# Optimization experiments

Hardware: AMD Instinct MI355X
Metric: run time of the kernel (lower is better)

The kernel has to match this reference:

```python
import jax, jax.numpy as jnp
import numpy as np

D_MODEL = 1024
NHEAD = 16
D_K = D_MODEL // NHEAD
D_FF = 4096
EPS = 1e-5


def _layer_norm(x, g, b):
    mu = jnp.mean(x, axis=-1, keepdims=True)
    var = jnp.mean(jnp.square(x - mu), axis=-1, keepdims=True)
    return (x - mu) * jax.lax.rsqrt(var + EPS) * g + b


def setup_inputs() -> dict:
    key = jax.random.key(0)
    ks = jax.random.split(key, 14)
    s = 0.02
    d = {
        'src': jax.random.normal(ks[0], (4, 2048, D_MODEL), dtype=jnp.float32),
        'Wq': jax.random.normal(ks[1], (D_MODEL, D_MODEL), dtype=jnp.float32) * s,
        'bq': jnp.zeros((D_MODEL,), jnp.float32),
        'Wk': jax.random.normal(ks[2], (D_MODEL, D_MODEL), dtype=jnp.float32) * s,
        'bk': jnp.zeros((D_MODEL,), jnp.float32),
        'Wv': jax.random.normal(ks[3], (D_MODEL, D_MODEL), dtype=jnp.float32) * s,
        'bv': jnp.zeros((D_MODEL,), jnp.float32),
        'Wo': jax.random.normal(ks[4], (D_MODEL, D_MODEL), dtype=jnp.float32) * s,
        'bo': jnp.zeros((D_MODEL,), jnp.float32),
        'W1': jax.random.normal(ks[5], (D_MODEL, D_FF), dtype=jnp.float32) * s,
        'b1': jnp.zeros((D_FF,), jnp.float32),
        'W2': jax.random.normal(ks[6], (D_FF, D_MODEL), dtype=jnp.float32) * s,
        'b2': jnp.zeros((D_MODEL,), jnp.float32),
        'ln1_g': jnp.ones((D_MODEL,), jnp.float32),
        'ln1_b': jnp.zeros((D_MODEL,), jnp.float32),
        'ln2_g': jnp.ones((D_MODEL,), jnp.float32),
        'ln2_b': jnp.zeros((D_MODEL,), jnp.float32),
    }
    return d


def reference(src, Wq, bq, Wk, bk, Wv, bv, Wo, bo, W1, b1, W2, b2,
              ln1_g, ln1_b, ln2_g, ln2_b):
    B, L, _ = src.shape
    # QKV projections -> [B, H, L, d_k]
    def heads(x, W, b):
        y = x @ W + b
        return y.reshape(B, L, NHEAD, D_K).transpose(0, 2, 1, 3)
    Q = heads(src, Wq, bq)
    K = heads(src, Wk, bk)
    V = heads(src, Wv, bv)
    # scores [B, H, Lq, Lk]
    scores = jnp.einsum('bhqd,bhkd->bhqk', Q, K) / jnp.sqrt(jnp.float32(D_K))
    attn = jax.nn.softmax(scores, axis=-1)
    ctx = jnp.einsum('bhqk,bhkd->bhqd', attn, V)
    ctx = ctx.transpose(0, 2, 1, 3).reshape(B, L, D_MODEL)
    attn_out = ctx @ Wo + bo
    x = _layer_norm(src + attn_out, ln1_g, ln1_b)
    ff = jax.nn.relu(x @ W1 + b1) @ W2 + b2
    return _layer_norm(x + ff, ln2_g, ln2_b)
```

## Files before the change

kernel.cpp:

```cpp
#include <hip/hip_runtime.h>
#include <hip/hip_bf16.h>


#define D_MODEL 1024
#define SEQ     2048
#define BATCH   4
#define NHEAD   16
#define D_FF    4096
#define M_ROWS  (BATCH * SEQ)

typedef __attribute__((ext_vector_type(8))) short bf16x8;
typedef __attribute__((ext_vector_type(4))) float f32x4;

__device__ __forceinline__ ushort f2bf(float x) {
    unsigned u = __float_as_uint(x);
    unsigned r = (u + 0x7FFFu + ((u >> 16) & 1u)) >> 16;
    return (ushort)r;
}

__device__ __forceinline__ int swz_off(int r, int q) {
    return ((r >> 1) << 6) | (((((r & 1) << 2) | q) ^ ((r >> 1) & 7)) << 3);
}

__global__ __launch_bounds__(256) void cast_kernel(
    const float* __restrict__ x, ushort* __restrict__ y)
{
    const size_t i = ((size_t)blockIdx.x * 256 + threadIdx.x) * 4;
    float4 v = *(const float4*)&x[i];
    ushort4 o;
    o.x = f2bf(v.x); o.y = f2bf(v.y); o.z = f2bf(v.z); o.w = f2bf(v.w);
    *(ushort4*)&y[i] = o;
}

__global__ __launch_bounds__(256) void transpose_cast_kernel(
    const float* __restrict__ W, ushort* __restrict__ Wt, int R, int C)
{
    __shared__ float tile[64][68];
    const int c0 = blockIdx.x * 64, r0 = blockIdx.y * 64;
    const int t  = threadIdx.x;
    const int tc  = (t & 15) * 4;
    const int tr4 = (t >> 4) * 4;
#pragma unroll
    for (int i = 0; i < 4; ++i) {
        float4 v = *(const float4*)&W[(size_t)(r0 + tr4 + i) * C + c0 + tc];
        *(float4*)&tile[tr4 + i][tc] = v;
    }
    __syncthreads();
#pragma unroll
    for (int i = 0; i < 4; ++i) {
        const int nn = tr4 + i;
        ushort4 o;
        o.x = f2bf(tile[tc + 0][nn]);
        o.y = f2bf(tile[tc + 1][nn]);
        o.z = f2bf(tile[tc + 2][nn]);
        o.w = f2bf(tile[tc + 3][nn]);
        *(ushort4*)&Wt[(size_t)(c0 + nn) * R + r0 + tc] = o;
    }
}

__global__ __launch_bounds__(256) void transpose_cast4_kernel(
    const float* __restrict__ Wq, const float* __restrict__ Wk,
    const float* __restrict__ Wv, const float* __restrict__ Wo,
    ushort* __restrict__ Wqkvt, ushort* __restrict__ Wot)
{
    const int z = blockIdx.z;
    const float* W = (z == 0) ? Wq : (z == 1) ? Wk : (z == 2) ? Wv : Wo;
    ushort* out = (z < 3) ? (Wqkvt + (size_t)z * 1024 * 1024) : Wot;

    __shared__ float tile[64][68];
    const int c0 = blockIdx.x * 64, r0 = blockIdx.y * 64;
    const int t  = threadIdx.x;
    const int tc  = (t & 15) * 4;
    const int tr4 = (t >> 4) * 4;
#pragma unroll
    for (int i = 0; i < 4; ++i) {
        float4 v = *(const float4*)&W[(size_t)(r0 + tr4 + i) * 1024 + c0 + tc];
        *(float4*)&tile[tr4 + i][tc] = v;
    }
    __syncthreads();
#pragma unroll
    for (int i = 0; i < 4; ++i) {
        const int nn = tr4 + i;
        ushort4 o;
        o.x = f2bf(tile[tc + 0][nn]);
        o.y = f2bf(tile[tc + 1][nn]);
        o.z = f2bf(tile[tc + 2][nn]);
        o.w = f2bf(tile[tc + 3][nn]);
        *(ushort4*)&out[(size_t)(c0 + nn) * 1024 + r0 + tc] = o;
    }
}

template <int MODE, int TM>
__global__ __launch_bounds__(256) void gemm_mfma(
    const ushort* __restrict__ A, const ushort* __restrict__ Bt,
    const float* __restrict__ bias0, const float* __restrict__ bias1,
    const float* __restrict__ bias2, void* __restrict__ C,
    int M, int N, int K, int nx)
{
    __shared__ __attribute__((aligned(16))) ushort As[TM * 32];
    __shared__ __attribute__((aligned(16))) ushort Bs[128 * 32];

    const int t    = threadIdx.x;
    const int lane = t & 63;
    const int wave = t >> 6;

    const int bid = blockIdx.y * gridDim.x + blockIdx.x;
    const int idx = bid >> 3;
    const int bxs = idx % nx;
    const int bys = (bid & 7) * (gridDim.y >> 3) + idx / nx;
    const int bm  = bys * TM;
    const int bn  = bxs * 128;

    constexpr int WI = TM / 32;
    const int wm   = (wave & 1) * (TM / 2);
    const int wn   = (wave >> 1) * 64;
    const int fr   = lane & 15;
    const int quad = lane >> 4;

    f32x4 acc[WI][4];
#pragma unroll
    for (int i = 0; i < WI; ++i)
#pragma unroll
        for (int j = 0; j < 4; ++j)
            acc[i][j] = (f32x4){0.f, 0.f, 0.f, 0.f};

    for (int k0 = 0; k0 < K; k0 += 32) {
#pragma unroll
        for (int r = 0; r < TM / 64; ++r) {
            const int s   = r * 256 + t;
            const int c   = (s & ~7) | ((s & 7) ^ ((s >> 3) & 7));
            const int row = c >> 2;
            const int kc  = (c & 3) * 8;
            __builtin_amdgcn_global_load_lds(
                (const __attribute__((address_space(1))) void*)(A + (size_t)(bm + row) * K + k0 + kc),
                (__attribute__((address_space(3))) void*)(As + s * 8), 16, 0, 0);
        }
#pragma unroll
        for (int r = 0; r < 2; ++r) {
            const int s   = r * 256 + t;
            const int c   = (s & ~7) | ((s & 7) ^ ((s >> 3) & 7));
            const int row = c >> 2;
            const int kc  = (c & 3) * 8;
            __builtin_amdgcn_global_load_lds(
                (const __attribute__((address_space(1))) void*)(Bt + (size_t)(bn + row) * K + k0 + kc),
                (__attribute__((address_space(3))) void*)(Bs + s * 8), 16, 0, 0);
        }
        __syncthreads();

        bf16x8 af[WI], bfr[4];
#pragma unroll
        for (int i = 0; i < WI; ++i)
            af[i] = *(const bf16x8*)&As[swz_off(wm + i * 16 + fr, quad)];
#pragma unroll
        for (int j = 0; j < 4; ++j)
            bfr[j] = *(const bf16x8*)&Bs[swz_off(wn + j * 16 + fr, quad)];

#pragma unroll
        for (int i = 0; i < WI; ++i)
#pragma unroll
            for (int j = 0; j < 4; ++j)
                acc[i][j] = __builtin_amdgcn_mfma_f32_16x16x32_bf16(af[i], bfr[j], acc[i][j], 0, 0, 0);
        __syncthreads();
    }

    const int rbase = quad * 4;
#pragma unroll
    for (int j = 0; j < 4; ++j) {
        const int col   = bn + wn + j * 16 + fr;
        const int third = (bn + wn + j * 16) >> 10;
        float bc;
        float sc = 1.f;
        if (MODE == 4) {
            const float* bp = (third == 0) ? bias0 : (third == 1) ? bias1 : bias2;
            bc = bp[col & 1023];
            if (third == 0) sc = 0.125f;
        } else {
            bc = bias0[col];
        }
#pragma unroll
        for (int i = 0; i < WI; ++i) {
            const int row0 = bm + wm + i * 16 + rbase;
            float v[4];
#pragma unroll
            for (int r = 0; r < 4; ++r) v[r] = (acc[i][j][r] + bc) * sc;

            if (MODE == 0) {
#pragma unroll
                for (int r = 0; r < 4; ++r)
                    ((float*)C)[(size_t)(row0 + r) * N + col] = v[r];
            } else if (MODE == 2) {
#pragma unroll
                for (int r = 0; r < 4; ++r)
                    ((ushort*)C)[(size_t)(row0 + r) * N + col] = f2bf(fmaxf(v[r], 0.f));
            } else {
                const int lc = col & 1023;
                const int h  = lc >> 6, d = lc & 63;
                if (third < 2) {
                    ushort* base = (ushort*)C + (size_t)third * 8 * 1024 * 1024;
#pragma unroll
                    for (int r = 0; r < 4; ++r) {
                        const int row = row0 + r;
                        const int b = row >> 11, l = row & 2047;
                        base[(((size_t)(b * NHEAD + h) * SEQ + l) << 6) + d] = f2bf(v[r]);
                    }
                } else {
                    ushort* base = (ushort*)C + (size_t)16 * 1024 * 1024;
                    const int b = row0 >> 11, l0 = row0 & 2047;
                    ushort4 o;
                    o.x = f2bf(v[0]); o.y = f2bf(v[1]); o.z = f2bf(v[2]); o.w = f2bf(v[3]);
                    *(ushort4*)&base[(((size_t)(b * NHEAD + h) * 64 + d) << 11) + l0] = o;
                }
            }
        }
    }
}

__global__ __launch_bounds__(256, 3) void attn_mfma(
    const ushort* __restrict__ Q, const ushort* __restrict__ K,
    const ushort* __restrict__ Vt, ushort* __restrict__ CTX)
{
    __shared__ __attribute__((aligned(16))) ushort Ks[64 * 64];
    __shared__ __attribute__((aligned(16))) ushort Vs[64 * 64];
    __shared__ __attribute__((aligned(16))) ushort Ps[128 * 64];

    const int t    = threadIdx.x;
    const int lane = t & 63;
    const int w    = t >> 6;
    const int l15  = lane & 15;
    const int quad = lane >> 4;

    const int bid = blockIdx.y * gridDim.x + blockIdx.x;
    const int idx = bid >> 3;
    const int bh  = (bid & 7) * 8 + (idx >> 4);
    const int q0  = (idx & 15) * 128;

    bf16x8 afq[2][2];
    const ushort* Qbase = Q + ((size_t)bh * SEQ + q0 + w * 32) * 64;
#pragma unroll
    for (int i = 0; i < 2; ++i)
#pragma unroll
        for (int ks = 0; ks < 2; ++ks)
            afq[i][ks] = *(const bf16x8*)&Qbase[(i * 16 + l15) * 64 + quad * 8 + ks * 32];

    f32x4 oacc[2][4];
#pragma unroll
    for (int i = 0; i < 2; ++i)
#pragma unroll
        for (int d = 0; d < 4; ++d) oacc[i][d] = (f32x4){0.f, 0.f, 0.f, 0.f};
    float lrun[2][4];
#pragma unroll
    for (int i = 0; i < 2; ++i)
#pragma unroll
        for (int r = 0; r < 4; ++r) lrun[i][r] = 0.f;

    const ushort* Kb  = K  + ((size_t)bh * SEQ) * 64;
    const ushort* Vtb = Vt + ((size_t)bh * 64) * SEQ;

    const int srow0 = t >> 3;
    const int sc8   = t & 7;

    for (int kk0 = 0; kk0 < SEQ; kk0 += 64) {
        bf16x8 kv0 = *(const bf16x8*)&Kb[(size_t)(kk0 + srow0) * 64 + sc8 * 8];
        bf16x8 kv1 = *(const bf16x8*)&Kb[(size_t)(kk0 + srow0 + 32) * 64 + sc8 * 8];
        bf16x8 vv0 = *(const bf16x8*)&Vtb[(size_t)srow0 * SEQ + kk0 + sc8 * 8];
        bf16x8 vv1 = *(const bf16x8*)&Vtb[(size_t)(srow0 + 32) * SEQ + kk0 + sc8 * 8];

        __syncthreads();

        {
            const int pr0 = (srow0 & 3) * 16 + (srow0 >> 2);
            const int pr1 = ((srow0 + 32) & 3) * 16 + ((srow0 + 32) >> 2);
            *(bf16x8*)&Ks[pr0 * 64 + ((sc8 ^ (pr0 & 7)) << 3)] = kv0;
            *(bf16x8*)&Ks[pr1 * 64 + ((sc8 ^ (pr1 & 7)) << 3)] = kv1;
            *(bf16x8*)&Vs[srow0 * 64 + ((sc8 ^ (srow0 & 7)) << 3)] = vv0;
            *(bf16x8*)&Vs[(srow0 + 32) * 64 + ((sc8 ^ ((srow0 + 32) & 7)) << 3)] = vv1;
        }
        __syncthreads();

        f32x4 sacc[2][4];
#pragma unroll
        for (int i = 0; i < 2; ++i)
#pragma unroll
            for (int j = 0; j < 4; ++j) sacc[i][j] = (f32x4){0.f, 0.f, 0.f, 0.f};
        const int swz0 = (quad ^ (l15 & 7)) << 3;
        const int swz1 = ((quad + 4) ^ (l15 & 7)) << 3;
#pragma unroll
        for (int j = 0; j < 4; ++j) {
            const int krow = (j * 16 + l15) * 64;
            bf16x8 bk0 = *(const bf16x8*)&Ks[krow + swz0];
            bf16x8 bk1 = *(const bf16x8*)&Ks[krow + swz1];
            sacc[0][j] = __builtin_amdgcn_mfma_f32_16x16x32_bf16(afq[0][0], bk0, sacc[0][j], 0, 0, 0);
            sacc[0][j] = __builtin_amdgcn_mfma_f32_16x16x32_bf16(afq[0][1], bk1, sacc[0][j], 0, 0, 0);
            sacc[1][j] = __builtin_amdgcn_mfma_f32_16x16x32_bf16(afq[1][0], bk0, sacc[1][j], 0, 0, 0);
            sacc[1][j] = __builtin_amdgcn_mfma_f32_16x16x32_bf16(afq[1][1], bk1, sacc[1][j], 0, 0, 0);
        }

#pragma unroll
        for (int i = 0; i < 2; ++i) {
#pragma unroll
            for (int r = 0; r < 4; ++r) {
                const float p0 = __expf(sacc[i][0][r]);
                const float p1 = __expf(sacc[i][1][r]);
                const float p2 = __expf(sacc[i][2][r]);
                const float p3 = __expf(sacc[i][3][r]);
                lrun[i][r] += (p0 + p1) + (p2 + p3);
                const unsigned u0 = __builtin_amdgcn_perm(
                    __float_as_uint(p1), __float_as_uint(p0), 0x07060302u);
                const unsigned u1 = __builtin_amdgcn_perm(
                    __float_as_uint(p3), __float_as_uint(p2), 0x07060302u);
                const int prow = w * 32 + i * 16 + quad * 4 + r;
                const int off = prow * 64 + (((l15 >> 1) ^ (prow & 7)) << 3) + (l15 & 1) * 4;
                *(unsigned long long*)&Ps[off] =
                    (unsigned long long)u0 | ((unsigned long long)u1 << 32);
            }
        }

        bf16x8 ap[2][2];
#pragma unroll
        for (int i = 0; i < 2; ++i) {
            const int prow = (w * 32 + i * 16 + l15) * 64;
            ap[i][0] = *(const bf16x8*)&Ps[prow + swz0];
            ap[i][1] = *(const bf16x8*)&Ps[prow + swz1];
        }
#pragma unroll
        for (int dt = 0; dt < 4; ++dt) {
            const int vrow = (dt * 16 + l15) * 64;
            bf16x8 bv0 = *(const bf16x8*)&Vs[vrow + swz0];
            bf16x8 bv1 = *(const bf16x8*)&Vs[vrow + swz1];
            oacc[0][dt] = __builtin_amdgcn_mfma_f32_16x16x32_bf16(ap[0][0], bv0, oacc[0][dt], 0, 0, 0);
            oacc[0][dt] = __builtin_amdgcn_mfma_f32_16x16x32_bf16(ap[0][1], bv1, oacc[0][dt], 0, 0, 0);
            oacc[1][dt] = __builtin_amdgcn_mfma_f32_16x16x32_bf16(ap[1][0], bv0, oacc[1][dt], 0, 0, 0);
            oacc[1][dt] = __builtin_amdgcn_mfma_f32_16x16x32_bf16(ap[1][1], bv1, oacc[1][dt], 0, 0, 0);
        }
    }

    const int b = bh >> 4, h = bh & 15;
#pragma unroll
    for (int i = 0; i < 2; ++i) {
#pragma unroll
        for (int r = 0; r < 4; ++r) {
            float l = lrun[i][r];
#pragma unroll
            for (int m = 1; m < 16; m <<= 1) l += __shfl_xor(l, m, 64);
            const float inv = 1.f / l;
            const int tok = q0 + w * 32 + i * 16 + quad * 4 + r;
            ushort* op = CTX + ((size_t)(b * SEQ + tok)) * D_MODEL + h * 64;
#pragma unroll
            for (int dt = 0; dt < 4; ++dt)
                op[dt * 16 + l15] = f2bf(oacc[i][dt][r] * inv);
        }
    }
}

template <bool WRITE_BF>
__global__ __launch_bounds__(256) void ln_kernel(
    const float* __restrict__ y, const float* __restrict__ res,
    const float* __restrict__ g, const float* __restrict__ bta,
    float* __restrict__ out, ushort* __restrict__ out_bf)
{
    __shared__ float red[4];
    const int t = threadIdx.x;
    const size_t base = (size_t)blockIdx.x * D_MODEL + t * 4;

    float4 a = *(const float4*)&y[base];
    float4 r = *(const float4*)&res[base];
    const float v0 = a.x + r.x, v1 = a.y + r.y, v2 = a.z + r.z, v3 = a.w + r.w;

    float s = v0 + v1 + v2 + v3;
#pragma unroll
    for (int o = 32; o > 0; o >>= 1) s += __shfl_down(s, o, 64);
    if ((t & 63) == 0) red[t >> 6] = s;
    __syncthreads();
    const float mu = (red[0] + red[1] + red[2] + red[3]) * (1.f / 1024.f);

    const float d0 = v0 - mu, d1 = v1 - mu, d2 = v2 - mu, d3 = v3 - mu;
    float sq = d0 * d0 + d1 * d1 + d2 * d2 + d3 * d3;
#pragma unroll
    for (int o = 32; o > 0; o >>= 1) sq += __shfl_down(sq, o, 64);
    __syncthreads();
    if ((t & 63) == 0) red[t >> 6] = sq;
    __syncthreads();
    const float var  = (red[0] + red[1] + red[2] + red[3]) * (1.f / 1024.f);
    const float rstd = rsqrtf(var + 1e-5f);

    const int c = t * 4;
    float4 gv = *(const float4*)&g[c];
    float4 bv = *(const float4*)&bta[c];
    float4 o4;
    o4.x = d0 * rstd * gv.x + bv.x;
    o4.y = d1 * rstd * gv.y + bv.y;
    o4.z = d2 * rstd * gv.z + bv.z;
    o4.w = d3 * rstd * gv.w + bv.w;
    *(float4*)&out[base] = o4;
    if (WRITE_BF) {
        ushort4 ob;
        ob.x = f2bf(o4.x); ob.y = f2bf(o4.y); ob.z = f2bf(o4.z); ob.w = f2bf(o4.w);
        *(ushort4*)&out_bf[base] = ob;
    }
}

extern "C" void kernel_launch(void* const* d_in, const int* in_sizes, int n_in,
                              void* d_out, int out_size, void* d_ws, size_t ws_size,
                              hipStream_t stream)
{
    const float* src = (const float*)d_in[0];
    const float* Wq  = (const float*)d_in[1];  const float* bq = (const float*)d_in[2];
    const float* Wk  = (const float*)d_in[3];  const float* bk = (const float*)d_in[4];
    const float* Wv  = (const float*)d_in[5];  const float* bv = (const float*)d_in[6];
    const float* Wo  = (const float*)d_in[7];  const float* bo = (const float*)d_in[8];
    const float* W1  = (const float*)d_in[9];  const float* b1 = (const float*)d_in[10];
    const float* W2  = (const float*)d_in[11]; const float* b2 = (const float*)d_in[12];
    const float* g1  = (const float*)d_in[13]; const float* be1 = (const float*)d_in[14];
    const float* g2  = (const float*)d_in[15]; const float* be2 = (const float*)d_in[16];
    float* out = (float*)d_out;

    char* ws = (char*)d_ws;
    const size_t MB = 1024 * 1024;
    ushort* Qb    = (ushort*)(ws);
    ushort* Kb    = (ushort*)(ws + 16 * MB);
    ushort* Vtb   = (ushort*)(ws + 32 * MB);
    ushort* CTXb  = (ushort*)(ws + 48 * MB);
    ushort* FFb   = (ushort*)(ws);
    float*  Xf    = (float*) (ws + 64 * MB);
    ushort* X1b   = (ushort*)(ws + 96 * MB);
    ushort* SRCb  = (ushort*)(ws + 112 * MB);
    ushort* W1t   = (ushort*)(ws + 112 * MB);
    ushort* W2t   = (ushort*)(ws + 120 * MB);
    ushort* Wqkvt = (ushort*)(ws + 128 * MB);
    ushort* Wot   = (ushort*)(ws + 134 * MB);

    dim3 blk(256);

    cast_kernel<<<dim3(M_ROWS * D_MODEL / 1024), blk, 0, stream>>>(src, SRCb);
    transpose_cast4_kernel<<<dim3(16, 16, 4), blk, 0, stream>>>(Wq, Wk, Wv, Wo, Wqkvt, Wot);

    gemm_mfma<4, 128><<<dim3(24, 64), blk, 0, stream>>>(
        SRCb, Wqkvt, bq, bk, bv, Qb, M_ROWS, 3 * D_MODEL, D_MODEL, 24);

    transpose_cast_kernel<<<dim3(64, 16), blk, 0, stream>>>(W1, W1t, D_MODEL, D_FF);
    transpose_cast_kernel<<<dim3(16, 64), blk, 0, stream>>>(W2, W2t, D_FF, D_MODEL);

    attn_mfma<<<dim3(SEQ / 128, BATCH * NHEAD), blk, 0, stream>>>(Qb, Kb, Vtb, CTXb);

    gemm_mfma<0, 64><<<dim3(8, 128), blk, 0, stream>>>(
        CTXb, Wot, bo, nullptr, nullptr, Xf, M_ROWS, D_MODEL, D_MODEL, 8);

    ln_kernel<true><<<M_ROWS, blk, 0, stream>>>(Xf, src, g1, be1, Xf, X1b);

    gemm_mfma<2, 128><<<dim3(32, 64), blk, 0, stream>>>(
        X1b, W1t, b1, nullptr, nullptr, FFb, M_ROWS, D_FF, D_MODEL, 32);

    gemm_mfma<0, 64><<<dim3(8, 128), blk, 0, stream>>>(
        FFb, W2t, b2, nullptr, nullptr, out, M_ROWS, D_MODEL, D_FF, 8);

    ln_kernel<false><<<M_ROWS, blk, 0, stream>>>(out, Xf, g2, be2, out, nullptr);
}
```

Measured before the change: 553.5 us.

## Load A fragments directly from global into registers with prefetch, unify 128-row tiles

The GEMM no longer stages the A tile through LDS. Each wave loads its A fragments straight from global memory into registers and prefetches the next k-step's fragments before the barrier, while B still goes through LDS. The template's TM parameter is removed, so the N=1024 GEMMs now use 128-row tiles with half as many blocks. This removes LDS traffic and a shared buffer, but the A reads become strided per-lane global loads with no cross-wave sharing, and the small GEMMs run with fewer blocks.

```diff
diff --git a/kernel.cpp b/kernel.cpp
--- a/kernel.cpp
+++ b/kernel.cpp
@@ -90,14 +90,13 @@
     }
 }
 
-template <int MODE, int TM>
+template <int MODE>
 __global__ __launch_bounds__(256) void gemm_mfma(
     const ushort* __restrict__ A, const ushort* __restrict__ Bt,
     const float* __restrict__ bias0, const float* __restrict__ bias1,
     const float* __restrict__ bias2, void* __restrict__ C,
     int M, int N, int K, int nx)
 {
-    __shared__ __attribute__((aligned(16))) ushort As[TM * 32];
     __shared__ __attribute__((aligned(16))) ushort Bs[128 * 32];
 
     const int t    = threadIdx.x;
@@ -108,33 +107,29 @@
     const int idx = bid >> 3;
     const int bxs = idx % nx;
     const int bys = (bid & 7) * (gridDim.y >> 3) + idx / nx;
-    const int bm  = bys * TM;
+    const int bm  = bys * 128;
     const int bn  = bxs * 128;
 
-    constexpr int WI = TM / 32;
-    const int wm   = (wave & 1) * (TM / 2);
+    const int wm   = (wave & 1) * 64;
     const int wn   = (wave >> 1) * 64;
     const int fr   = lane & 15;
     const int quad = lane >> 4;
 
-    f32x4 acc[WI][4];
-#pragma unroll
-    for (int i = 0; i < WI; ++i)
+    f32x4 acc[4][4];
+#pragma unroll
+    for (int i = 0; i < 4; ++i)
 #pragma unroll
         for (int j = 0; j < 4; ++j)
             acc[i][j] = (f32x4){0.f, 0.f, 0.f, 0.f};
 
+    const ushort* Ap = A + (size_t)(bm + wm + fr) * K + quad * 8;
+
+    bf16x8 afn[4];
+#pragma unroll
+    for (int i = 0; i < 4; ++i)
+        afn[i] = *(const bf16x8*)(Ap + (size_t)(i * 16) * K);
+
     for (int k0 = 0; k0 < K; k0 += 32) {
-#pragma unroll
-        for (int r = 0; r < TM / 64; ++r) {
-            const int s   = r * 256 + t;
-            const int c   = (s & ~7) | ((s & 7) ^ ((s >> 3) & 7));
-            const int row = c >> 2;
-            const int kc  = (c & 3) * 8;
-            __builtin_amdgcn_global_load_lds(
-                (const __attribute__((address_space(1))) void*)(A + (size_t)(bm + row) * K + k0 + kc),
-                (__attribute__((address_space(3))) void*)(As + s * 8), 16, 0, 0);
-        }
 #pragma unroll
         for (int r = 0; r < 2; ++r) {
             const int s   = r * 256 + t;
@@ -145,18 +140,26 @@
                 (const __attribute__((address_space(1))) void*)(Bt + (size_t)(bn + row) * K + k0 + kc),
                 (__attribute__((address_space(3))) void*)(Bs + s * 8), 16, 0, 0);
         }
+
+        bf16x8 af[4];
+#pragma unroll
+        for (int i = 0; i < 4; ++i) af[i] = afn[i];
+        const int kn = k0 + 32;
+        if (kn < K) {
+#pragma unroll
+            for (int i = 0; i < 4; ++i)
+                afn[i] = *(const bf16x8*)(Ap + (size_t)(i * 16) * K + kn);
+        }
+
         __syncthreads();
 
-        bf16x8 af[WI], bfr[4];
-#pragma unroll
-        for (int i = 0; i < WI; ++i)
-            af[i] = *(const bf16x8*)&As[swz_off(wm + i * 16 + fr, quad)];
+        bf16x8 bfr[4];
 #pragma unroll
         for (int j = 0; j < 4; ++j)
             bfr[j] = *(const bf16x8*)&Bs[swz_off(wn + j * 16 + fr, quad)];
 
 #pragma unroll
-        for (int i = 0; i < WI; ++i)
+        for (int i = 0; i < 4; ++i)
 #pragma unroll
             for (int j = 0; j < 4; ++j)
                 acc[i][j] = __builtin_amdgcn_mfma_f32_16x16x32_bf16(af[i], bfr[j], acc[i][j], 0, 0, 0);
@@ -178,7 +181,7 @@
             bc = bias0[col];
         }
 #pragma unroll
-        for (int i = 0; i < WI; ++i) {
+        for (int i = 0; i < 4; ++i) {
             const int row0 = bm + wm + i * 16 + rbase;
             float v[4];
 #pragma unroll
@@ -434,7 +437,7 @@
     cast_kernel<<<dim3(M_ROWS * D_MODEL / 1024), blk, 0, stream>>>(src, SRCb);
     transpose_cast4_kernel<<<dim3(16, 16, 4), blk, 0, stream>>>(Wq, Wk, Wv, Wo, Wqkvt, Wot);
 
-    gemm_mfma<4, 128><<<dim3(24, 64), blk, 0, stream>>>(
+    gemm_mfma<4><<<dim3(24, 64), blk, 0, stream>>>(
         SRCb, Wqkvt, bq, bk, bv, Qb, M_ROWS, 3 * D_MODEL, D_MODEL, 24);
 
     transpose_cast_kernel<<<dim3(64, 16), blk, 0, stream>>>(W1, W1t, D_MODEL, D_FF);
@@ -442,15 +445,15 @@
 
     attn_mfma<<<dim3(SEQ / 128, BATCH * NHEAD), blk, 0, stream>>>(Qb, Kb, Vtb, CTXb);
 
-    gemm_mfma<0, 64><<<dim3(8, 128), blk, 0, stream>>>(
+    gemm_mfma<0><<<dim3(8, 64), blk, 0, stream>>>(
         CTXb, Wot, bo, nullptr, nullptr, Xf, M_ROWS, D_MODEL, D_MODEL, 8);
 
     ln_kernel<true><<<M_ROWS, blk, 0, stream>>>(Xf, src, g1, be1, Xf, X1b);
 
-    gemm_mfma<2, 128><<<dim3(32, 64), blk, 0, stream>>>(
+    gemm_mfma<2><<<dim3(32, 64), blk, 0, stream>>>(
         X1b, W1t, b1, nullptr, nullptr, FFb, M_ROWS, D_FF, D_MODEL, 32);
 
-    gemm_mfma<0, 64><<<dim3(8, 128), blk, 0, stream>>>(
+    gemm_mfma<0><<<dim3(8, 64), blk, 0, stream>>>(
         FFb, W2t, b2, nullptr, nullptr, out, M_ROWS, D_MODEL, D_FF, 8);
 
     ln_kernel<false><<<M_ROWS, blk, 0, stream>>>(out, Xf, g2, be2, out, nullptr);
```

Result: slower. 696.3 us (+25.8%).
